# Kernel tuning notes

Hardware: AMD Instinct MI355X
Metric: run time of the kernel (lower is better)

## Reference

```python
import jax, jax.numpy as jnp
import numpy as np

NUM_MODELS = 4
B = 16384
HIDDEN = 512
QDIM = 256
LAST_HIDDEN = 256
UW = 0.1          # uncertainty_weight
EPS = 1e-5        # LayerNorm eps (torch default)
FEAT_DIMS = [1024, 768, 512, 640]


def _linear(x, W, b):
    return x @ W.T + b


def _layernorm(h, g, b):
    mu = jnp.mean(h, axis=-1, keepdims=True)
    var = jnp.mean((h - mu) ** 2, axis=-1, keepdims=True)
    return (h - mu) * jax.lax.rsqrt(var + EPS) * g + b


def setup_inputs() -> dict:
    key = jax.random.key(0)
    ks = jax.random.split(key, 40)
    inp = {}
    for i, d in enumerate(FEAT_DIMS):
        inp[f"feat{i}"] = jax.random.normal(ks[i], (B, d), jnp.float32)
        inp[f"W_intra{i}"] = jax.random.normal(ks[4 + i], (HIDDEN, d), jnp.float32) / np.sqrt(d)
        inp[f"b_intra{i}"] = jnp.zeros((HIDDEN,), jnp.float32)
    inp["pred_scores"] = jax.random.uniform(ks[8], (B, NUM_MODELS), jnp.float32)
    inp["pred_vars"] = jax.random.uniform(ks[9], (B, NUM_MODELS), jnp.float32)
    inp["ln_g"] = jnp.ones((HIDDEN,), jnp.float32)
    inp["ln_b"] = jnp.zeros((HIDDEN,), jnp.float32)
    inp["Wq"] = jax.random.normal(ks[10], (QDIM, HIDDEN), jnp.float32) / np.sqrt(HIDDEN)
    inp["bq"] = jnp.zeros((QDIM,), jnp.float32)
    inp["Wk"] = jax.random.normal(ks[11], (QDIM, HIDDEN), jnp.float32) / np.sqrt(HIDDEN)
    inp["bk"] = jnp.zeros((QDIM,), jnp.float32)
    inp["Wv"] = jax.random.normal(ks[12], (QDIM, HIDDEN), jnp.float32) / np.sqrt(HIDDEN)
    inp["bv"] = jnp.zeros((QDIM,), jnp.float32)
    d1 = NUM_MODELS * QDIM + NUM_MODELS
    inp["W1"] = jax.random.normal(ks[13], (LAST_HIDDEN, d1), jnp.float32) / np.sqrt(d1)
    inp["b1"] = jnp.zeros((LAST_HIDDEN,), jnp.float32)
    inp["Wfc"] = jax.random.normal(ks[14], (1, LAST_HIDDEN), jnp.float32) / np.sqrt(LAST_HIDDEN)
    inp["bfc"] = jnp.zeros((1,), jnp.float32)
    return inp


def _forward(feats, pred_scores, pred_vars, W_intras, b_intras,
             ln_g, ln_b, Wq, bq, Wk, bk, Wv, bv, W1, b1, Wfc, bfc):
    # per-model branch: Linear -> ReLU -> (dropout=id) -> ReLU -> LayerNorm
    hiddens = []
    for i in range(NUM_MODELS):
        h = jax.nn.relu(_linear(feats[i], W_intras[i], b_intras[i]))
        h = jax.nn.relu(h)  # second relu after dropout (identity in eval)
        hiddens.append(_layernorm(h, ln_g, ln_b))
    H = jnp.stack(hiddens, axis=1)  # (B, M, HIDDEN)

    # cross-attention with uncertainty; NOTE source bug: key = drop(q) => keys == queries
    q = jnp.einsum('bmh,qh->bmq', H, Wq) + bq          # (B, M, Q)
    k = q                                              # faithful to `key = self.drop(q)`
    v = jnp.einsum('bmh,qh->bmq', H, Wv) + bv          # (B, M, Q)

    scores = jnp.einsum('biq,bjq->bij', q, k)          # (B, M, M)
    vars_ = pred_vars[:, None, :] + pred_vars[:, :, None]  # vars[b,i,j] = v[b,j] + v[b,i]
    scores = jax.nn.softmax(scores - UW * vars_, axis=-1)
    z = jnp.einsum('bij,bjq->biq', scores, v).reshape(B, NUM_MODELS * QDIM)

    out = jnp.concatenate([z, pred_scores], axis=-1)
    out = _linear(out, W1, b1)
    logits = _linear(out, Wfc, bfc)
    return jax.nn.sigmoid(logits)  # (B, 1)


def reference(feat0, feat1, feat2, feat3,
              W_intra0, b_intra0, W_intra1, b_intra1,
              W_intra2, b_intra2, W_intra3, b_intra3,
              pred_scores, pred_vars, ln_g, ln_b,
              Wq, bq, Wk, bk, Wv, bv, W1, b1, Wfc, bfc):
    feats = [feat0, feat1, feat2, feat3]
    W_intras = [W_intra0, W_intra1, W_intra2, W_intra3]
    b_intras = [b_intra0, b_intra1, b_intra2, b_intra3]
    return _forward(feats, pred_scores, pred_vars, W_intras, b_intras,
                    ln_g, ln_b, Wq, bq, Wk, bk, Wv, bv, W1, b1, Wfc, bfc)
```

## Files before the change

kernel.cpp:

```cpp
#include <hip/hip_runtime.h>
#include <hip/hip_bf16.h>


typedef __bf16 bf16;
typedef __bf16 bf16x4_t __attribute__((ext_vector_type(4)));
typedef __bf16 bf16x8_t __attribute__((ext_vector_type(8)));
typedef float  f32x4_t  __attribute__((ext_vector_type(4)));

__device__ __forceinline__ bf16x8_t cvt8(f32x4_t a, f32x4_t b) {
  bf16x8_t r;
  r[0] = (bf16)a[0]; r[1] = (bf16)a[1]; r[2] = (bf16)a[2]; r[3] = (bf16)a[3];
  r[4] = (bf16)b[0]; r[5] = (bf16)b[1]; r[6] = (bf16)b[2]; r[7] = (bf16)b[3];
  return r;
}

__device__ __forceinline__ void gl_lds16(const void* g, void* l) {
  __builtin_amdgcn_global_load_lds(
      (const __attribute__((address_space(1))) void*)g,
      (__attribute__((address_space(3))) void*)l, 16, 0, 0);
}

__device__ __forceinline__ bf16x8_t frag_read(const bf16* Ts, int row, int c0) {
  const int byte = row * 64 + ((c0 ^ ((row >> 1) & 3)) << 4);
  return *(const bf16x8_t*)((const char*)Ts + byte);
}

__device__ __forceinline__ void stage_b16(const bf16* __restrict__ src, int ld,
                                          int k0, bf16* lds) {
  const int l = threadIdx.x & 63;
  const int w = threadIdx.x >> 6;
#pragma unroll
  for (int j = 0; j < 2; ++j) {
    const int rb = w * 32 + j * 16;
    const int r  = rb + (l >> 2);
    const int sc = (l & 3) ^ ((r >> 1) & 3);
    gl_lds16(src + (size_t)r * ld + k0 + sc * 8, (char*)lds + rb * 64);
  }
}

__device__ __forceinline__ void stage_b512(const bf16* __restrict__ src, int ld,
                                           int k0, bf16* lds) {
  const int l = threadIdx.x & 63;
  const int w = threadIdx.x >> 6;
#pragma unroll
  for (int j = 0; j < 8; ++j) {
    const int rb = w * 128 + j * 16;
    const int r  = rb + (l >> 2);
    const int sc = (l & 3) ^ ((r >> 1) & 3);
    gl_lds16(src + (size_t)r * ld + k0 + sc * 8, (char*)lds + rb * 64);
  }
}

__device__ __forceinline__ void commit2(const f32x4_t v[4], bf16* lds,
                                        int srow, int shalf) {
  const int sw = (srow >> 1) & 3;
  *(bf16x8_t*)((char*)lds + srow * 64 + (((shalf * 2)     ^ sw) << 4)) = cvt8(v[0], v[1]);
  *(bf16x8_t*)((char*)lds + srow * 64 + (((shalf * 2 + 1) ^ sw) << 4)) = cvt8(v[2], v[3]);
}

__device__ __forceinline__ void mfma_step(const bf16* As, const bf16* Bs,
                                          f32x4_t acc[4][4]) {
  const int lane = threadIdx.x & 63;
  const int wid  = threadIdx.x >> 6;
  const int wm = wid >> 1, wn = wid & 1;
  const int fr = lane & 15, c0 = lane >> 4;
  bf16x8_t ar[4], br[4];
#pragma unroll
  for (int mi = 0; mi < 4; ++mi) ar[mi] = frag_read(As, wm * 64 + mi * 16 + fr, c0);
#pragma unroll
  for (int ni = 0; ni < 4; ++ni) br[ni] = frag_read(Bs, wn * 64 + ni * 16 + fr, c0);
#pragma unroll
  for (int mi = 0; mi < 4; ++mi)
#pragma unroll
    for (int ni = 0; ni < 4; ++ni)
      acc[mi][ni] = __builtin_amdgcn_mfma_f32_16x16x32_bf16(ar[mi], br[ni], acc[mi][ni], 0, 0, 0);
}

__device__ __forceinline__ void mfma_step8(const bf16* As, const bf16* Bs,
                                           f32x4_t acc[4][8]) {
  const int lane = threadIdx.x & 63;
  const int wn   = threadIdx.x >> 6;
  const int fr = lane & 15, c0 = lane >> 4;
  bf16x8_t ar[4], br[8];
#pragma unroll
  for (int mi = 0; mi < 4; ++mi) ar[mi] = frag_read(As, mi * 16 + fr, c0);
#pragma unroll
  for (int ni = 0; ni < 8; ++ni) br[ni] = frag_read(Bs, wn * 128 + ni * 16 + fr, c0);
#pragma unroll
  for (int mi = 0; mi < 4; ++mi)
#pragma unroll
    for (int ni = 0; ni < 8; ++ni)
      acc[mi][ni] = __builtin_amdgcn_mfma_f32_16x16x32_bf16(ar[mi], br[ni], acc[mi][ni], 0, 0, 0);
}

#define WAIT_VM6()  asm volatile("s_waitcnt vmcnt(6)" ::: "memory")
#define WAIT_VM10() asm volatile("s_waitcnt vmcnt(10)" ::: "memory")
#define WAIT_VM0()  asm volatile("s_waitcnt vmcnt(0)" ::: "memory")
#define WAIT_LGKM() asm volatile("s_waitcnt lgkmcnt(0)" ::: "memory")
#define SBAR()      __builtin_amdgcn_s_barrier()
#define SCHED0()    __builtin_amdgcn_sched_barrier(0)

template<int REG_IS_A>
__device__ __forceinline__ void core_db(
    const float* __restrict__ regsrc, int rld,
    const bf16* __restrict__ dmasrc, int dld, int K,
    bf16* R0, bf16* R1, bf16* D0, bf16* D1, f32x4_t acc[4][4])
{
  const int tid  = threadIdx.x;
  const int srow = tid >> 1, shalf = tid & 1;
  const float* Rf = regsrc + (size_t)srow * rld + shalf * 16;

  f32x4_t ra[4], rb[4];
#pragma unroll
  for (int i = 0; i < 4; ++i) ra[i] = *(const f32x4_t*)(Rf + i * 4);
  stage_b16(dmasrc, dld, 0, D0);

  for (int k0 = 0; k0 < K; k0 += 64) {
    stage_b16(dmasrc, dld, k0 + 32, D1);
#pragma unroll
    for (int i = 0; i < 4; ++i) rb[i] = *(const f32x4_t*)(Rf + k0 + 32 + i * 4);
    WAIT_VM6();
    commit2(ra, R0, srow, shalf);
    WAIT_LGKM();
    SBAR(); SCHED0();
    if (REG_IS_A) mfma_step(R0, D0, acc); else mfma_step(D0, R0, acc);
    SCHED0(); SBAR();
    if (k0 + 64 < K) {
      stage_b16(dmasrc, dld, k0 + 64, D0);
#pragma unroll
      for (int i = 0; i < 4; ++i) ra[i] = *(const f32x4_t*)(Rf + k0 + 64 + i * 4);
      WAIT_VM6();
    } else {
      WAIT_VM0();
    }
    commit2(rb, R1, srow, shalf);
    WAIT_LGKM();
    SBAR(); SCHED0();
    if (REG_IS_A) mfma_step(R1, D1, acc); else mfma_step(D1, R1, acc);
    SCHED0(); SBAR();
  }
}

template<int RELU>
__device__ __forceinline__ void epi_bf16(f32x4_t acc[4][4], bf16* __restrict__ C, int ldc,
                                         const float* __restrict__ bias) {
  const int lane = threadIdx.x & 63;
  const int wid  = threadIdx.x >> 6;
  const int wm = wid >> 1, wn = wid & 1;
  const int fr = lane & 15;
  const int rb = wm * 64 + 4 * (lane >> 4);
  const int cb = wn * 64 + fr;
  float bv[4];
#pragma unroll
  for (int ni = 0; ni < 4; ++ni) bv[ni] = bias[cb + ni * 16];
#pragma unroll
  for (int mi = 0; mi < 4; ++mi)
#pragma unroll
    for (int j = 0; j < 4; ++j)
#pragma unroll
      for (int ni = 0; ni < 4; ++ni) {
        float val = acc[mi][ni][j] + bv[ni];
        if (RELU) val = fmaxf(val, 0.f);
        C[(size_t)(rb + mi * 16 + j) * ldc + cb + ni * 16] = (bf16)val;
      }
}

__device__ __forceinline__ void cp8(bf16* d, const float* s) {
  f32x4_t x0 = *(const f32x4_t*)s;
  f32x4_t x1 = *(const f32x4_t*)(s + 4);
  *(bf16x8_t*)d = cvt8(x0, x1);
}

__global__ __launch_bounds__(256) void prep_kernel(
    const float* __restrict__ w0, const float* __restrict__ w1s,
    const float* __restrict__ w2, const float* __restrict__ w3,
    bf16* __restrict__ o0, bf16* __restrict__ o1,
    bf16* __restrict__ o2, bf16* __restrict__ o3) {
  const int t = blockIdx.x * 256 + threadIdx.x;
  if (t < 65536)       { size_t i = (size_t)t * 8;            cp8(o0 + i, w0 + i); }
  else if (t < 114688) { size_t i = (size_t)(t - 65536) * 8;  cp8(o1 + i, w1s + i); }
  else if (t < 147456) { size_t i = (size_t)(t - 114688) * 8; cp8(o2 + i, w2 + i); }
  else                 { size_t i = (size_t)(t - 147456) * 8; cp8(o3 + i, w3 + i); }
}

__global__ __launch_bounds__(256, 2) void intra_ln_kernel(
    const float* __restrict__ f0, const float* __restrict__ f1,
    const float* __restrict__ f2, const float* __restrict__ f3,
    const bf16* __restrict__ wb0, const bf16* __restrict__ wb1,
    const bf16* __restrict__ wb2, const bf16* __restrict__ wb3,
    const float* __restrict__ bb0, const float* __restrict__ bb1,
    const float* __restrict__ bb2, const float* __restrict__ bb3,
    const float* __restrict__ lng, const float* __restrict__ lnb,
    bf16* __restrict__ Hout) {
  __shared__ __align__(16) char smem[73728];
  bf16* B0 = (bf16*)smem;
  bf16* B1 = (bf16*)(smem + 32768);
  bf16* A0 = (bf16*)(smem + 65536);
  bf16* A1 = (bf16*)(smem + 69632);
  bf16* hl = (bf16*)smem;

  const int bid = blockIdx.x;
  const int lid = (bid & 7) * 128 + (bid >> 3);
  const int z = lid & 3;
  const int y = lid >> 2;
  const float* fp; const bf16* wp; const float* bp; int K;
  switch (z) {
    case 0:  fp = f0; wp = wb0; bp = bb0; K = 1024; break;
    case 1:  fp = f1; wp = wb1; bp = bb1; K = 768;  break;
    case 2:  fp = f2; wp = wb2; bp = bb2; K = 512;  break;
    default: fp = f3; wp = wb3; bp = bb3; K = 640;  break;
  }
  const int tid  = threadIdx.x;
  const int lane = tid & 63;
  const int wn   = tid >> 6;
  const int srow = tid >> 2, sq = tid & 3;
  const float* Af = fp + (size_t)(y * 64 + srow) * K + sq * 8;
  const int abyte = srow * 64 + ((sq ^ ((srow >> 1) & 3)) << 4);

  f32x4_t acc[4][8];
#pragma unroll
  for (int i = 0; i < 4; ++i)
#pragma unroll
    for (int j = 0; j < 8; ++j) acc[i][j] = (f32x4_t){0.f, 0.f, 0.f, 0.f};

  f32x4_t ra0, ra1, rb0, rb1;
  ra0 = *(const f32x4_t*)(Af + 0);  ra1 = *(const f32x4_t*)(Af + 4);
  stage_b512(wp, K, 0, B0);

  for (int k0 = 0; k0 < K; k0 += 64) {
    stage_b512(wp, K, k0 + 32, B1);
    rb0 = *(const f32x4_t*)(Af + k0 + 32);  rb1 = *(const f32x4_t*)(Af + k0 + 36);
    WAIT_VM10();
    { f32x4_t v[1]; (void)v; }
    *(bf16x8_t*)((char*)A0 + abyte) = cvt8(ra0, ra1);
    WAIT_LGKM();
    SBAR(); SCHED0();
    mfma_step8(A0, B0, acc);
    SCHED0(); SBAR();
    if (k0 + 64 < K) {
      stage_b512(wp, K, k0 + 64, B0);
      ra0 = *(const f32x4_t*)(Af + k0 + 64);  ra1 = *(const f32x4_t*)(Af + k0 + 68);
      WAIT_VM10();
    } else {
      WAIT_VM0();
    }
    *(bf16x8_t*)((char*)A1 + abyte) = cvt8(rb0, rb1);
    WAIT_LGKM();
    SBAR(); SCHED0();
    mfma_step8(A1, B1, acc);
    SCHED0(); SBAR();
  }

  const int fr = lane & 15;
  const int rbase = 4 * (lane >> 4);
  const int cb = wn * 128 + fr;
  float bv[8];
#pragma unroll
  for (int ni = 0; ni < 8; ++ni) bv[ni] = bp[cb + ni * 16];
#pragma unroll
  for (int mi = 0; mi < 4; ++mi)
#pragma unroll
    for (int j = 0; j < 4; ++j) {
      const int row = mi * 16 + rbase + j;
#pragma unroll
      for (int ni = 0; ni < 8; ++ni) {
        float v = fmaxf(acc[mi][ni][j] + bv[ni], 0.f);
        hl[row * 512 + cb + ni * 16] = (bf16)v;
      }
    }
  __syncthreads();

  f32x4_t g0 = *(const f32x4_t*)(lng + lane * 8);
  f32x4_t g1 = *(const f32x4_t*)(lng + lane * 8 + 4);
  f32x4_t be0 = *(const f32x4_t*)(lnb + lane * 8);
  f32x4_t be1 = *(const f32x4_t*)(lnb + lane * 8 + 4);
#pragma unroll
  for (int r16 = 0; r16 < 16; ++r16) {
    const int row = wn * 16 + r16;
    const bf16x8_t xv = *(const bf16x8_t*)(hl + row * 512 + lane * 8);
    float xf[8]; float s = 0.f, s2 = 0.f;
#pragma unroll
    for (int j = 0; j < 8; ++j) { xf[j] = (float)xv[j]; s += xf[j]; s2 += xf[j] * xf[j]; }
#pragma unroll
    for (int off = 1; off < 64; off <<= 1) { s += __shfl_xor(s, off); s2 += __shfl_xor(s2, off); }
    const float mu  = s * (1.f / 512.f);
    const float var = s2 * (1.f / 512.f) - mu * mu;
    const float inv = rsqrtf(var + 1e-5f);
    bf16x8_t o;
#pragma unroll
    for (int j = 0; j < 4; ++j) o[j]     = (bf16)((xf[j] - mu) * inv * g0[j] + be0[j]);
#pragma unroll
    for (int j = 0; j < 4; ++j) o[4 + j] = (bf16)((xf[4 + j] - mu) * inv * g1[j] + be1[j]);
    *(bf16x8_t*)(Hout + (size_t)(y * 64 + row) * 2048 + z * 512 + lane * 8) = o;
  }
}

__global__ __launch_bounds__(256) void qv_kernel(
    const bf16* __restrict__ H, const float* __restrict__ Wq,
    const float* __restrict__ Wv, const float* __restrict__ bq,
    const float* __restrict__ bv, bf16* __restrict__ qvout) {
  __shared__ bf16 A0[128 * 32], A1[128 * 32], B0[128 * 32], B1[128 * 32];
  const int bid = blockIdx.x;
  const int lid = (bid & 7) * 256 + (bid >> 3);
  const int x = lid & 3, y = lid >> 2;
  const float* Wsrc = (x < 2) ? Wq : Wv;
  f32x4_t acc[4][4];
#pragma unroll
  for (int i = 0; i < 4; ++i)
#pragma unroll
    for (int j = 0; j < 4; ++j) acc[i][j] = (f32x4_t){0.f, 0.f, 0.f, 0.f};
  core_db<0>(Wsrc + (size_t)((x & 1) * 128) * 512, 512,
             H + (size_t)(y * 128) * 512, 512, 512, B0, B1, A0, A1, acc);
  const float* bias = (x < 2) ? bq + x * 128 : bv + (x - 2) * 128;
  epi_bf16<0>(acc, qvout + (size_t)(y * 128) * 512 + x * 128, 512, bias);
}

__global__ __launch_bounds__(256) void w1_kernel(
    const bf16* __restrict__ zb, const float* __restrict__ W1,
    const float* __restrict__ b1, const float* __restrict__ ps,
    float* __restrict__ obuf) {
  __shared__ bf16 A0[128 * 32], A1[128 * 32], B0[128 * 32], B1[128 * 32];
  const int bid = blockIdx.x;
  const int lid = (bid & 7) * 32 + (bid >> 3);
  const int x = lid & 1, y = lid >> 1;
  f32x4_t acc[4][4];
#pragma unroll
  for (int i = 0; i < 4; ++i)
#pragma unroll
    for (int j = 0; j < 4; ++j) acc[i][j] = (f32x4_t){0.f, 0.f, 0.f, 0.f};
  core_db<0>(W1 + (size_t)(x * 128) * 1028, 1028,
             zb + (size_t)(y * 128) * 1024, 1024, 1024, B0, B1, A0, A1, acc);

  const int lane = threadIdx.x & 63;
  const int wid  = threadIdx.x >> 6;
  const int wm = wid >> 1, wn = wid & 1;
  const int fr = lane & 15;
  const int rb = wm * 64 + 4 * (lane >> 4);
  const int cb = x * 128 + wn * 64 + fr;
  float bv[4], wt[4][4];
#pragma unroll
  for (int ni = 0; ni < 4; ++ni) {
    bv[ni] = b1[cb + ni * 16];
#pragma unroll
    for (int m = 0; m < 4; ++m) wt[ni][m] = W1[(size_t)(cb + ni * 16) * 1028 + 1024 + m];
  }
#pragma unroll
  for (int mi = 0; mi < 4; ++mi)
#pragma unroll
    for (int j = 0; j < 4; ++j) {
      const int r = y * 128 + rb + mi * 16 + j;
      f32x4_t psv = *(const f32x4_t*)(ps + (size_t)r * 4);
#pragma unroll
      for (int ni = 0; ni < 4; ++ni) {
        float val = acc[mi][ni][j] + bv[ni]
                  + psv[0] * wt[ni][0] + psv[1] * wt[ni][1]
                  + psv[2] * wt[ni][2] + psv[3] * wt[ni][3];
        obuf[(size_t)r * 256 + cb + ni * 16] = val;
      }
    }
}

__global__ __launch_bounds__(256)
void attn_kernel(const bf16* __restrict__ qv, const float* __restrict__ pvars,
                 bf16* __restrict__ z) {
  const int b    = blockIdx.x * 4 + (threadIdx.x >> 6);
  const int lane = threadIdx.x & 63;
  float qf[4][4], vf[4][4];
#pragma unroll
  for (int i = 0; i < 4; ++i) {
    const bf16* row = qv + ((size_t)b * 4 + i) * 512;
    bf16x4_t qq = *(const bf16x4_t*)(row + lane * 4);
    bf16x4_t vv = *(const bf16x4_t*)(row + 256 + lane * 4);
#pragma unroll
    for (int c = 0; c < 4; ++c) { qf[i][c] = (float)qq[c]; vf[i][c] = (float)vv[c]; }
  }
  float s[4][4];
#pragma unroll
  for (int i = 0; i < 4; ++i)
#pragma unroll
    for (int j = 0; j < 4; ++j)
      s[i][j] = qf[i][0] * qf[j][0] + qf[i][1] * qf[j][1] + qf[i][2] * qf[j][2] + qf[i][3] * qf[j][3];
#pragma unroll
  for (int off = 1; off < 64; off <<= 1)
#pragma unroll
    for (int i = 0; i < 4; ++i)
#pragma unroll
      for (int j = 0; j < 4; ++j) s[i][j] += __shfl_xor(s[i][j], off);

  float var4[4];
#pragma unroll
  for (int m = 0; m < 4; ++m) var4[m] = pvars[(size_t)b * 4 + m];
  float w[4][4];
#pragma unroll
  for (int i = 0; i < 4; ++i) {
    float t[4]; float mx = -1e30f;
#pragma unroll
    for (int j = 0; j < 4; ++j) { t[j] = s[i][j] - 0.1f * (var4[i] + var4[j]); mx = fmaxf(mx, t[j]); }
    float sum = 0.f;
#pragma unroll
    for (int j = 0; j < 4; ++j) { t[j] = expf(t[j] - mx); sum += t[j]; }
    const float is = 1.f / sum;
#pragma unroll
    for (int j = 0; j < 4; ++j) w[i][j] = t[j] * is;
  }
#pragma unroll
  for (int i = 0; i < 4; ++i) {
    bf16x4_t zo;
#pragma unroll
    for (int c = 0; c < 4; ++c) {
      float zf = w[i][0] * vf[0][c] + w[i][1] * vf[1][c] + w[i][2] * vf[2][c] + w[i][3] * vf[3][c];
      zo[c] = (bf16)zf;
    }
    *(bf16x4_t*)(z + ((size_t)b * 4 + i) * 256 + lane * 4) = zo;
  }
}

__global__ __launch_bounds__(256)
void fc_kernel(const float* __restrict__ o, const float* __restrict__ wfc,
               const float* __restrict__ bfc, float* __restrict__ out) {
  const int b    = blockIdx.x * 4 + (threadIdx.x >> 6);
  const int lane = threadIdx.x & 63;
  f32x4_t ov = *(const f32x4_t*)(o + (size_t)b * 256 + lane * 4);
  f32x4_t wv = *(const f32x4_t*)(wfc + lane * 4);
  float p = ov[0] * wv[0] + ov[1] * wv[1] + ov[2] * wv[2] + ov[3] * wv[3];
#pragma unroll
  for (int off = 1; off < 64; off <<= 1) p += __shfl_xor(p, off);
  if (lane == 0) {
    const float lg = p + bfc[0];
    out[b] = 1.f / (1.f + expf(-lg));
  }
}

extern "C" void kernel_launch(void* const* d_in, const int* in_sizes, int n_in,
                              void* d_out, int out_size, void* d_ws, size_t ws_size,
                              hipStream_t stream) {
  (void)in_sizes; (void)n_in; (void)out_size; (void)ws_size;
  const float* feat[4] = {(const float*)d_in[0], (const float*)d_in[3],
                          (const float*)d_in[6], (const float*)d_in[9]};
  const float* Wi[4]   = {(const float*)d_in[1], (const float*)d_in[4],
                          (const float*)d_in[7], (const float*)d_in[10]};
  const float* bi[4]   = {(const float*)d_in[2], (const float*)d_in[5],
                          (const float*)d_in[8], (const float*)d_in[11]};
  const float* ps  = (const float*)d_in[12];
  const float* pv  = (const float*)d_in[13];
  const float* lng = (const float*)d_in[14];
  const float* lnb = (const float*)d_in[15];
  const float* Wq  = (const float*)d_in[16];
  const float* bq  = (const float*)d_in[17];
  const float* Wv  = (const float*)d_in[20];
  const float* bvp = (const float*)d_in[21];
  const float* W1  = (const float*)d_in[22];
  const float* b1  = (const float*)d_in[23];
  const float* Wfc = (const float*)d_in[24];
  const float* bfc = (const float*)d_in[25];

  char* ws = (char*)d_ws;
  const size_t MB = 1024 * 1024;
  bf16*  Hbuf  = (bf16*)ws;
  bf16*  zbuf  = (bf16*)ws;
  float* obuf  = (float*)(ws + 32 * MB);
  bf16*  wb0   = (bf16*)(ws + 64 * MB);
  bf16*  wb1   = (bf16*)(ws + 65 * MB);
  bf16*  wb2   = (bf16*)(ws + 65 * MB + 786432);
  bf16*  wb3   = (bf16*)(ws + 66 * MB + 262144);
  bf16*  qvout = (bf16*)(ws + 64 * MB);

  hipLaunchKernelGGL(prep_kernel, dim3(736), dim3(256), 0, stream,
                     Wi[0], Wi[1], Wi[2], Wi[3], wb0, wb1, wb2, wb3);
  hipLaunchKernelGGL(intra_ln_kernel, dim3(1024), dim3(256), 0, stream,
                     feat[0], feat[1], feat[2], feat[3],
                     wb0, wb1, wb2, wb3, bi[0], bi[1], bi[2], bi[3],
                     lng, lnb, Hbuf);
  hipLaunchKernelGGL(qv_kernel, dim3(2048), dim3(256), 0, stream,
                     Hbuf, Wq, Wv, bq, bvp, qvout);
  hipLaunchKernelGGL(attn_kernel, dim3(16384 / 4), dim3(256), 0, stream, qvout, pv, zbuf);
  hipLaunchKernelGGL(w1_kernel, dim3(256), dim3(256), 0, stream, zbuf, W1, b1, ps, obuf);
  hipLaunchKernelGGL(fc_kernel, dim3(16384 / 4), dim3(256), 0, stream, obuf, Wfc, bfc, (float*)d_out);
}
```

Measured before the change: 255.4 us.

## Fuse Q/V projection into intra-branch LayerNorm kernel with register-held B fragments

Merges the per-model linear+ReLU+LayerNorm kernel with the Q/V projection so the normalized hidden tile stays in LDS (XOR-swizzled) and is consumed directly as the A operand, removing the H round trip through global memory and one launch. The B operand (weights) is now loaded straight from global into registers instead of being staged through LDS, shrinking shared memory. Wq/Wv are pre-converted to bf16 in the prep kernel. Risks include higher register pressure with two sets of B fragments, uncoalesced-ish direct global B loads, and a longer serial kernel per block.

```diff
diff --git a/kernel.cpp b/kernel.cpp
--- a/kernel.cpp
+++ b/kernel.cpp
@@ -25,144 +25,49 @@
   return *(const bf16x8_t*)((const char*)Ts + byte);
 }
 
-__device__ __forceinline__ void stage_b16(const bf16* __restrict__ src, int ld,
-                                          int k0, bf16* lds) {
-  const int l = threadIdx.x & 63;
-  const int w = threadIdx.x >> 6;
-#pragma unroll
-  for (int j = 0; j < 2; ++j) {
-    const int rb = w * 32 + j * 16;
-    const int r  = rb + (l >> 2);
-    const int sc = (l & 3) ^ ((r >> 1) & 3);
-    gl_lds16(src + (size_t)r * ld + k0 + sc * 8, (char*)lds + rb * 64);
-  }
-}
-
-__device__ __forceinline__ void stage_b512(const bf16* __restrict__ src, int ld,
-                                           int k0, bf16* lds) {
-  const int l = threadIdx.x & 63;
-  const int w = threadIdx.x >> 6;
-#pragma unroll
-  for (int j = 0; j < 8; ++j) {
-    const int rb = w * 128 + j * 16;
-    const int r  = rb + (l >> 2);
-    const int sc = (l & 3) ^ ((r >> 1) & 3);
-    gl_lds16(src + (size_t)r * ld + k0 + sc * 8, (char*)lds + rb * 64);
-  }
-}
-
-__device__ __forceinline__ void commit2(const f32x4_t v[4], bf16* lds,
-                                        int srow, int shalf) {
-  const int sw = (srow >> 1) & 3;
-  *(bf16x8_t*)((char*)lds + srow * 64 + (((shalf * 2)     ^ sw) << 4)) = cvt8(v[0], v[1]);
-  *(bf16x8_t*)((char*)lds + srow * 64 + (((shalf * 2 + 1) ^ sw) << 4)) = cvt8(v[2], v[3]);
-}
-
-__device__ __forceinline__ void mfma_step(const bf16* As, const bf16* Bs,
-                                          f32x4_t acc[4][4]) {
-  const int lane = threadIdx.x & 63;
-  const int wid  = threadIdx.x >> 6;
-  const int wm = wid >> 1, wn = wid & 1;
-  const int fr = lane & 15, c0 = lane >> 4;
-  bf16x8_t ar[4], br[4];
-#pragma unroll
-  for (int mi = 0; mi < 4; ++mi) ar[mi] = frag_read(As, wm * 64 + mi * 16 + fr, c0);
-#pragma unroll
-  for (int ni = 0; ni < 4; ++ni) br[ni] = frag_read(Bs, wn * 64 + ni * 16 + fr, c0);
-#pragma unroll
-  for (int mi = 0; mi < 4; ++mi)
-#pragma unroll
-    for (int ni = 0; ni < 4; ++ni)
-      acc[mi][ni] = __builtin_amdgcn_mfma_f32_16x16x32_bf16(ar[mi], br[ni], acc[mi][ni], 0, 0, 0);
-}
-
-__device__ __forceinline__ void mfma_step8(const bf16* As, const bf16* Bs,
-                                           f32x4_t acc[4][8]) {
-  const int lane = threadIdx.x & 63;
-  const int wn   = threadIdx.x >> 6;
-  const int fr = lane & 15, c0 = lane >> 4;
-  bf16x8_t ar[4], br[8];
-#pragma unroll
-  for (int mi = 0; mi < 4; ++mi) ar[mi] = frag_read(As, mi * 16 + fr, c0);
-#pragma unroll
-  for (int ni = 0; ni < 8; ++ni) br[ni] = frag_read(Bs, wn * 128 + ni * 16 + fr, c0);
-#pragma unroll
-  for (int mi = 0; mi < 4; ++mi)
-#pragma unroll
-    for (int ni = 0; ni < 8; ++ni)
-      acc[mi][ni] = __builtin_amdgcn_mfma_f32_16x16x32_bf16(ar[mi], br[ni], acc[mi][ni], 0, 0, 0);
-}
-
 #define WAIT_VM6()  asm volatile("s_waitcnt vmcnt(6)" ::: "memory")
-#define WAIT_VM10() asm volatile("s_waitcnt vmcnt(10)" ::: "memory")
 #define WAIT_VM0()  asm volatile("s_waitcnt vmcnt(0)" ::: "memory")
 #define WAIT_LGKM() asm volatile("s_waitcnt lgkmcnt(0)" ::: "memory")
 #define SBAR()      __builtin_amdgcn_s_barrier()
 #define SCHED0()    __builtin_amdgcn_sched_barrier(0)
 
-template<int REG_IS_A>
-__device__ __forceinline__ void core_db(
-    const float* __restrict__ regsrc, int rld,
-    const bf16* __restrict__ dmasrc, int dld, int K,
-    bf16* R0, bf16* R1, bf16* D0, bf16* D1, f32x4_t acc[4][4])
-{
-  const int tid  = threadIdx.x;
-  const int srow = tid >> 1, shalf = tid & 1;
-  const float* Rf = regsrc + (size_t)srow * rld + shalf * 16;
-
-  f32x4_t ra[4], rb[4];
-#pragma unroll
-  for (int i = 0; i < 4; ++i) ra[i] = *(const f32x4_t*)(Rf + i * 4);
-  stage_b16(dmasrc, dld, 0, D0);
-
-  for (int k0 = 0; k0 < K; k0 += 64) {
-    stage_b16(dmasrc, dld, k0 + 32, D1);
-#pragma unroll
-    for (int i = 0; i < 4; ++i) rb[i] = *(const f32x4_t*)(Rf + k0 + 32 + i * 4);
-    WAIT_VM6();
-    commit2(ra, R0, srow, shalf);
-    WAIT_LGKM();
-    SBAR(); SCHED0();
-    if (REG_IS_A) mfma_step(R0, D0, acc); else mfma_step(D0, R0, acc);
-    SCHED0(); SBAR();
-    if (k0 + 64 < K) {
-      stage_b16(dmasrc, dld, k0 + 64, D0);
-#pragma unroll
-      for (int i = 0; i < 4; ++i) ra[i] = *(const f32x4_t*)(Rf + k0 + 64 + i * 4);
-      WAIT_VM6();
-    } else {
-      WAIT_VM0();
-    }
-    commit2(rb, R1, srow, shalf);
-    WAIT_LGKM();
-    SBAR(); SCHED0();
-    if (REG_IS_A) mfma_step(R1, D1, acc); else mfma_step(D1, R1, acc);
-    SCHED0(); SBAR();
-  }
-}
-
-template<int RELU>
-__device__ __forceinline__ void epi_bf16(f32x4_t acc[4][4], bf16* __restrict__ C, int ldc,
-                                         const float* __restrict__ bias) {
-  const int lane = threadIdx.x & 63;
-  const int wid  = threadIdx.x >> 6;
-  const int wm = wid >> 1, wn = wid & 1;
-  const int fr = lane & 15;
-  const int rb = wm * 64 + 4 * (lane >> 4);
-  const int cb = wn * 64 + fr;
-  float bv[4];
-#pragma unroll
-  for (int ni = 0; ni < 4; ++ni) bv[ni] = bias[cb + ni * 16];
+__device__ __forceinline__ void loadB8(const bf16* __restrict__ base, int ld,
+                                       int k0, bf16x8_t br[8]) {
+#pragma unroll
+  for (int ni = 0; ni < 8; ++ni)
+    br[ni] = *(const bf16x8_t*)(base + (size_t)ni * 16 * ld + k0);
+}
+
+__device__ __forceinline__ void mfma_regB(const bf16* As, const bf16x8_t br[8],
+                                          f32x4_t acc[4][8]) {
+  const int lane = threadIdx.x & 63;
+  const int fr = lane & 15, c0 = lane >> 4;
+  bf16x8_t ar[4];
+#pragma unroll
+  for (int mi = 0; mi < 4; ++mi) ar[mi] = frag_read(As, mi * 16 + fr, c0);
 #pragma unroll
   for (int mi = 0; mi < 4; ++mi)
 #pragma unroll
-    for (int j = 0; j < 4; ++j)
-#pragma unroll
-      for (int ni = 0; ni < 4; ++ni) {
-        float val = acc[mi][ni][j] + bv[ni];
-        if (RELU) val = fmaxf(val, 0.f);
-        C[(size_t)(rb + mi * 16 + j) * ldc + cb + ni * 16] = (bf16)val;
-      }
+    for (int ni = 0; ni < 8; ++ni)
+      acc[mi][ni] = __builtin_amdgcn_mfma_f32_16x16x32_bf16(ar[mi], br[ni], acc[mi][ni], 0, 0, 0);
+}
+
+__device__ __forceinline__ void mfma_hA(const bf16* h, int kc, const bf16x8_t br[8],
+                                        f32x4_t acc[4][8]) {
+  const int lane = threadIdx.x & 63;
+  const int fr = lane & 15, g = lane >> 4;
+  bf16x8_t ar[4];
+#pragma unroll
+  for (int mi = 0; mi < 4; ++mi) {
+    const int row = mi * 16 + fr;
+    const int byte = row * 1024 + (((kc + g) ^ (row & 7)) << 4);
+    ar[mi] = *(const bf16x8_t*)((const char*)h + byte);
+  }
+#pragma unroll
+  for (int mi = 0; mi < 4; ++mi)
+#pragma unroll
+    for (int ni = 0; ni < 8; ++ni)
+      acc[mi][ni] = __builtin_amdgcn_mfma_f32_16x16x32_bf16(ar[mi], br[ni], acc[mi][ni], 0, 0, 0);
 }
 
 __device__ __forceinline__ void cp8(bf16* d, const float* s) {
@@ -174,16 +79,19 @@
 __global__ __launch_bounds__(256) void prep_kernel(
     const float* __restrict__ w0, const float* __restrict__ w1s,
     const float* __restrict__ w2, const float* __restrict__ w3,
-    bf16* __restrict__ o0, bf16* __restrict__ o1,
-    bf16* __restrict__ o2, bf16* __restrict__ o3) {
+    const float* __restrict__ wq, const float* __restrict__ wv,
+    bf16* __restrict__ o0, bf16* __restrict__ o1, bf16* __restrict__ o2,
+    bf16* __restrict__ o3, bf16* __restrict__ oqv) {
   const int t = blockIdx.x * 256 + threadIdx.x;
   if (t < 65536)       { size_t i = (size_t)t * 8;            cp8(o0 + i, w0 + i); }
   else if (t < 114688) { size_t i = (size_t)(t - 65536) * 8;  cp8(o1 + i, w1s + i); }
   else if (t < 147456) { size_t i = (size_t)(t - 114688) * 8; cp8(o2 + i, w2 + i); }
-  else                 { size_t i = (size_t)(t - 147456) * 8; cp8(o3 + i, w3 + i); }
-}
-
-__global__ __launch_bounds__(256, 2) void intra_ln_kernel(
+  else if (t < 188416) { size_t i = (size_t)(t - 147456) * 8; cp8(o3 + i, w3 + i); }
+  else                 { int u = t - 188416; size_t i = (size_t)u * 8;
+                         cp8(oqv + i, (u < 16384) ? wq + i : wv + (i - 131072)); }
+}
+
+__global__ __launch_bounds__(256, 2) void mega_kernel(
     const float* __restrict__ f0, const float* __restrict__ f1,
     const float* __restrict__ f2, const float* __restrict__ f3,
     const bf16* __restrict__ wb0, const bf16* __restrict__ wb1,
@@ -191,13 +99,11 @@
     const float* __restrict__ bb0, const float* __restrict__ bb1,
     const float* __restrict__ bb2, const float* __restrict__ bb3,
     const float* __restrict__ lng, const float* __restrict__ lnb,
-    bf16* __restrict__ Hout) {
-  __shared__ __align__(16) char smem[73728];
-  bf16* B0 = (bf16*)smem;
-  bf16* B1 = (bf16*)(smem + 32768);
-  bf16* A0 = (bf16*)(smem + 65536);
-  bf16* A1 = (bf16*)(smem + 69632);
-  bf16* hl = (bf16*)smem;
+    const bf16* __restrict__ wqv, const float* __restrict__ bq,
+    const float* __restrict__ bv, bf16* __restrict__ qvout) {
+  __shared__ bf16 A0[64 * 32];
+  __shared__ bf16 A1[64 * 32];
+  __shared__ bf16 h[64 * 512];
 
   const int bid = blockIdx.x;
   const int lid = (bid & 7) * 128 + (bid >> 3);
@@ -213,9 +119,11 @@
   const int tid  = threadIdx.x;
   const int lane = tid & 63;
   const int wn   = tid >> 6;
+  const int fr   = lane & 15, g = lane >> 4;
   const int srow = tid >> 2, sq = tid & 3;
   const float* Af = fp + (size_t)(y * 64 + srow) * K + sq * 8;
   const int abyte = srow * 64 + ((sq ^ ((srow >> 1) & 3)) << 4);
+  const bf16* Bbase = wp + (size_t)(wn * 128 + fr) * K + g * 8;
 
   f32x4_t acc[4][8];
 #pragma unroll
@@ -224,95 +132,188 @@
     for (int j = 0; j < 8; ++j) acc[i][j] = (f32x4_t){0.f, 0.f, 0.f, 0.f};
 
   f32x4_t ra0, ra1, rb0, rb1;
+  bf16x8_t bc[8], bn[8];
   ra0 = *(const f32x4_t*)(Af + 0);  ra1 = *(const f32x4_t*)(Af + 4);
-  stage_b512(wp, K, 0, B0);
+  loadB8(Bbase, K, 0, bc);
 
   for (int k0 = 0; k0 < K; k0 += 64) {
-    stage_b512(wp, K, k0 + 32, B1);
+    loadB8(Bbase, K, k0 + 32, bn);
     rb0 = *(const f32x4_t*)(Af + k0 + 32);  rb1 = *(const f32x4_t*)(Af + k0 + 36);
-    WAIT_VM10();
-    { f32x4_t v[1]; (void)v; }
     *(bf16x8_t*)((char*)A0 + abyte) = cvt8(ra0, ra1);
     WAIT_LGKM();
     SBAR(); SCHED0();
-    mfma_step8(A0, B0, acc);
+    mfma_regB(A0, bc, acc);
     SCHED0(); SBAR();
     if (k0 + 64 < K) {
-      stage_b512(wp, K, k0 + 64, B0);
+      loadB8(Bbase, K, k0 + 64, bc);
       ra0 = *(const f32x4_t*)(Af + k0 + 64);  ra1 = *(const f32x4_t*)(Af + k0 + 68);
-      WAIT_VM10();
-    } else {
-      WAIT_VM0();
     }
     *(bf16x8_t*)((char*)A1 + abyte) = cvt8(rb0, rb1);
     WAIT_LGKM();
     SBAR(); SCHED0();
-    mfma_step8(A1, B1, acc);
+    mfma_regB(A1, bn, acc);
     SCHED0(); SBAR();
   }
 
-  const int fr = lane & 15;
-  const int rbase = 4 * (lane >> 4);
-  const int cb = wn * 128 + fr;
-  float bv[8];
-#pragma unroll
-  for (int ni = 0; ni < 8; ++ni) bv[ni] = bp[cb + ni * 16];
+  const int g4 = 4 * g;
+  {
+    float bv8[8];
+#pragma unroll
+    for (int ni = 0; ni < 8; ++ni) bv8[ni] = bp[wn * 128 + ni * 16 + fr];
+#pragma unroll
+    for (int mi = 0; mi < 4; ++mi)
+#pragma unroll
+      for (int j = 0; j < 4; ++j) {
+        const int row = mi * 16 + g4 + j;
+#pragma unroll
+        for (int ni = 0; ni < 8; ++ni) {
+          const int col = wn * 128 + ni * 16 + fr;
+          const int hb = row * 1024 + (((col >> 3) ^ (row & 7)) << 4) + (col & 7) * 2;
+          float v = fmaxf(acc[mi][ni][j] + bv8[ni], 0.f);
+          *(bf16*)((char*)h + hb) = (bf16)v;
+        }
+      }
+  }
+  __syncthreads();
+
+  {
+    f32x4_t gg0 = *(const f32x4_t*)(lng + lane * 8);
+    f32x4_t gg1 = *(const f32x4_t*)(lng + lane * 8 + 4);
+    f32x4_t be0 = *(const f32x4_t*)(lnb + lane * 8);
+    f32x4_t be1 = *(const f32x4_t*)(lnb + lane * 8 + 4);
+#pragma unroll
+    for (int r16 = 0; r16 < 16; ++r16) {
+      const int row = wn * 16 + r16;
+      const int hb = row * 1024 + ((lane ^ (row & 7)) << 4);
+      const bf16x8_t xv = *(const bf16x8_t*)((const char*)h + hb);
+      float xf[8]; float s = 0.f, s2 = 0.f;
+#pragma unroll
+      for (int j = 0; j < 8; ++j) { xf[j] = (float)xv[j]; s += xf[j]; s2 += xf[j] * xf[j]; }
+#pragma unroll
+      for (int off = 1; off < 64; off <<= 1) { s += __shfl_xor(s, off); s2 += __shfl_xor(s2, off); }
+      const float mu  = s * (1.f / 512.f);
+      const float var = s2 * (1.f / 512.f) - mu * mu;
+      const float inv = rsqrtf(var + 1e-5f);
+      bf16x8_t o;
+#pragma unroll
+      for (int j = 0; j < 4; ++j) o[j]     = (bf16)((xf[j] - mu) * inv * gg0[j] + be0[j]);
+#pragma unroll
+      for (int j = 0; j < 4; ++j) o[4 + j] = (bf16)((xf[4 + j] - mu) * inv * gg1[j] + be1[j]);
+      *(bf16x8_t*)((char*)h + hb) = o;
+    }
+  }
+  __syncthreads();
+
+#pragma unroll
+  for (int i = 0; i < 4; ++i)
+#pragma unroll
+    for (int j = 0; j < 8; ++j) acc[i][j] = (f32x4_t){0.f, 0.f, 0.f, 0.f};
+  const bf16* Qbase = wqv + (size_t)(wn * 128 + fr) * 512 + g * 8;
+  bf16x8_t qc[8], qn[8];
+  loadB8(Qbase, 512, 0, qc);
+  for (int k0 = 0; k0 < 512; k0 += 64) {
+    loadB8(Qbase, 512, k0 + 32, qn);
+    mfma_hA(h, k0 >> 3, qc, acc);
+    if (k0 + 64 < 512) loadB8(Qbase, 512, k0 + 64, qc);
+    mfma_hA(h, (k0 + 32) >> 3, qn, acc);
+  }
+
+  {
+    float bv8[8];
+#pragma unroll
+    for (int ni = 0; ni < 8; ++ni) {
+      const int col = wn * 128 + ni * 16 + fr;
+      bv8[ni] = (col < 256) ? bq[col] : bv[col - 256];
+    }
+#pragma unroll
+    for (int mi = 0; mi < 4; ++mi)
+#pragma unroll
+      for (int j = 0; j < 4; ++j) {
+        const int row = mi * 16 + g4 + j;
+        bf16* outp = qvout + ((size_t)(y * 64 + row) * 4 + z) * 512;
+#pragma unroll
+        for (int ni = 0; ni < 8; ++ni) {
+          const int col = wn * 128 + ni * 16 + fr;
+          outp[col] = (bf16)(acc[mi][ni][j] + bv8[ni]);
+        }
+      }
+  }
+}
+
+__device__ __forceinline__ void stage_b16(const bf16* __restrict__ src, int ld,
+                                          int k0, bf16* lds) {
+  const int l = threadIdx.x & 63;
+  const int w = threadIdx.x >> 6;
+#pragma unroll
+  for (int j = 0; j < 2; ++j) {
+    const int rb = w * 32 + j * 16;
+    const int r  = rb + (l >> 2);
+    const int sc = (l & 3) ^ ((r >> 1) & 3);
+    gl_lds16(src + (size_t)r * ld + k0 + sc * 8, (char*)lds + rb * 64);
+  }
+}
+
+__device__ __forceinline__ void commit2(const f32x4_t v[4], bf16* lds,
+                                        int srow, int shalf) {
+  const int sw = (srow >> 1) & 3;
+  *(bf16x8_t*)((char*)lds + srow * 64 + (((shalf * 2)     ^ sw) << 4)) = cvt8(v[0], v[1]);
+  *(bf16x8_t*)((char*)lds + srow * 64 + (((shalf * 2 + 1) ^ sw) << 4)) = cvt8(v[2], v[3]);
+}
+
+__device__ __forceinline__ void mfma_step(const bf16* As, const bf16* Bs,
+                                          f32x4_t acc[4][4]) {
+  const int lane = threadIdx.x & 63;
+  const int wid  = threadIdx.x >> 6;
+  const int wm = wid >> 1, wn = wid & 1;
+  const int fr = lane & 15, c0 = lane >> 4;
+  bf16x8_t ar[4], br[4];
+#pragma unroll
+  for (int mi = 0; mi < 4; ++mi) ar[mi] = frag_read(As, wm * 64 + mi * 16 + fr, c0);
+#pragma unroll
+  for (int ni = 0; ni < 4; ++ni) br[ni] = frag_read(Bs, wn * 64 + ni * 16 + fr, c0);
 #pragma unroll
   for (int mi = 0; mi < 4; ++mi)
 #pragma unroll
-    for (int j = 0; j < 4; ++j) {
-      const int row = mi * 16 + rbase + j;
-#pragma unroll
-      for (int ni = 0; ni < 8; ++ni) {
-        float v = fmaxf(acc[mi][ni][j] + bv[ni], 0.f);
-        hl[row * 512 + cb + ni * 16] = (bf16)v;
-      }
-    }
-  __syncthreads();
-
-  f32x4_t g0 = *(const f32x4_t*)(lng + lane * 8);
-  f32x4_t g1 = *(const f32x4_t*)(lng + lane * 8 + 4);
-  f32x4_t be0 = *(const f32x4_t*)(lnb + lane * 8);
-  f32x4_t be1 = *(const f32x4_t*)(lnb + lane * 8 + 4);
-#pragma unroll
-  for (int r16 = 0; r16 < 16; ++r16) {
-    const int row = wn * 16 + r16;
-    const bf16x8_t xv = *(const bf16x8_t*)(hl + row * 512 + lane * 8);
-    float xf[8]; float s = 0.f, s2 = 0.f;
-#pragma unroll
-    for (int j = 0; j < 8; ++j) { xf[j] = (float)xv[j]; s += xf[j]; s2 += xf[j] * xf[j]; }
-#pragma unroll
-    for (int off = 1; off < 64; off <<= 1) { s += __shfl_xor(s, off); s2 += __shfl_xor(s2, off); }
-    const float mu  = s * (1.f / 512.f);
-    const float var = s2 * (1.f / 512.f) - mu * mu;
-    const float inv = rsqrtf(var + 1e-5f);
-    bf16x8_t o;
-#pragma unroll
-    for (int j = 0; j < 4; ++j) o[j]     = (bf16)((xf[j] - mu) * inv * g0[j] + be0[j]);
-#pragma unroll
-    for (int j = 0; j < 4; ++j) o[4 + j] = (bf16)((xf[4 + j] - mu) * inv * g1[j] + be1[j]);
-    *(bf16x8_t*)(Hout + (size_t)(y * 64 + row) * 2048 + z * 512 + lane * 8) = o;
-  }
-}
-
-__global__ __launch_bounds__(256) void qv_kernel(
-    const bf16* __restrict__ H, const float* __restrict__ Wq,
-    const float* __restrict__ Wv, const float* __restrict__ bq,
-    const float* __restrict__ bv, bf16* __restrict__ qvout) {
-  __shared__ bf16 A0[128 * 32], A1[128 * 32], B0[128 * 32], B1[128 * 32];
-  const int bid = blockIdx.x;
-  const int lid = (bid & 7) * 256 + (bid >> 3);
-  const int x = lid & 3, y = lid >> 2;
-  const float* Wsrc = (x < 2) ? Wq : Wv;
-  f32x4_t acc[4][4];
-#pragma unroll
-  for (int i = 0; i < 4; ++i)
-#pragma unroll
-    for (int j = 0; j < 4; ++j) acc[i][j] = (f32x4_t){0.f, 0.f, 0.f, 0.f};
-  core_db<0>(Wsrc + (size_t)((x & 1) * 128) * 512, 512,
-             H + (size_t)(y * 128) * 512, 512, 512, B0, B1, A0, A1, acc);
-  const float* bias = (x < 2) ? bq + x * 128 : bv + (x - 2) * 128;
-  epi_bf16<0>(acc, qvout + (size_t)(y * 128) * 512 + x * 128, 512, bias);
+    for (int ni = 0; ni < 4; ++ni)
+      acc[mi][ni] = __builtin_amdgcn_mfma_f32_16x16x32_bf16(ar[mi], br[ni], acc[mi][ni], 0, 0, 0);
+}
+
+__device__ __forceinline__ void core_db0(
+    const float* __restrict__ regsrc, int rld,
+    const bf16* __restrict__ dmasrc, int dld, int K,
+    bf16* R0, bf16* R1, bf16* D0, bf16* D1, f32x4_t acc[4][4])
+{
+  const int tid  = threadIdx.x;
+  const int srow = tid >> 1, shalf = tid & 1;
+  const float* Rf = regsrc + (size_t)srow * rld + shalf * 16;
+  f32x4_t ra[4], rb[4];
+#pragma unroll
+  for (int i = 0; i < 4; ++i) ra[i] = *(const f32x4_t*)(Rf + i * 4);
+  stage_b16(dmasrc, dld, 0, D0);
+  for (int k0 = 0; k0 < K; k0 += 64) {
+    stage_b16(dmasrc, dld, k0 + 32, D1);
+#pragma unroll
+    for (int i = 0; i < 4; ++i) rb[i] = *(const f32x4_t*)(Rf + k0 + 32 + i * 4);
+    WAIT_VM6();
+    commit2(ra, R0, srow, shalf);
+    WAIT_LGKM();
+    SBAR(); SCHED0();
+    mfma_step(D0, R0, acc);
+    SCHED0(); SBAR();
+    if (k0 + 64 < K) {
+      stage_b16(dmasrc, dld, k0 + 64, D0);
+#pragma unroll
+      for (int i = 0; i < 4; ++i) ra[i] = *(const f32x4_t*)(Rf + k0 + 64 + i * 4);
+      WAIT_VM6();
+    } else {
+      WAIT_VM0();
+    }
+    commit2(rb, R1, srow, shalf);
+    WAIT_LGKM();
+    SBAR(); SCHED0();
+    mfma_step(D1, R1, acc);
+    SCHED0(); SBAR();
+  }
 }
 
 __global__ __launch_bounds__(256) void w1_kernel(
@@ -328,8 +329,8 @@
   for (int i = 0; i < 4; ++i)
 #pragma unroll
     for (int j = 0; j < 4; ++j) acc[i][j] = (f32x4_t){0.f, 0.f, 0.f, 0.f};
-  core_db<0>(W1 + (size_t)(x * 128) * 1028, 1028,
-             zb + (size_t)(y * 128) * 1024, 1024, 1024, B0, B1, A0, A1, acc);
+  core_db0(W1 + (size_t)(x * 128) * 1028, 1028,
+           zb + (size_t)(y * 128) * 1024, 1024, 1024, B0, B1, A0, A1, acc);
 
   const int lane = threadIdx.x & 63;
   const int wid  = threadIdx.x >> 6;
@@ -456,23 +457,22 @@
 
   char* ws = (char*)d_ws;
   const size_t MB = 1024 * 1024;
-  bf16*  Hbuf  = (bf16*)ws;
-  bf16*  zbuf  = (bf16*)ws;
-  float* obuf  = (float*)(ws + 32 * MB);
-  bf16*  wb0   = (bf16*)(ws + 64 * MB);
-  bf16*  wb1   = (bf16*)(ws + 65 * MB);
-  bf16*  wb2   = (bf16*)(ws + 65 * MB + 786432);
-  bf16*  wb3   = (bf16*)(ws + 66 * MB + 262144);
+  bf16*  wb0   = (bf16*)(ws);
+  bf16*  wb1   = (bf16*)(ws + 1048576);
+  bf16*  wb2   = (bf16*)(ws + 1835008);
+  bf16*  wb3   = (bf16*)(ws + 2359296);
+  bf16*  wqv   = (bf16*)(ws + 3014656);
+  bf16*  zbuf  = (bf16*)(ws + 8 * MB);
+  float* obuf  = (float*)(ws + 40 * MB);
   bf16*  qvout = (bf16*)(ws + 64 * MB);
 
-  hipLaunchKernelGGL(prep_kernel, dim3(736), dim3(256), 0, stream,
-                     Wi[0], Wi[1], Wi[2], Wi[3], wb0, wb1, wb2, wb3);
-  hipLaunchKernelGGL(intra_ln_kernel, dim3(1024), dim3(256), 0, stream,
+  hipLaunchKernelGGL(prep_kernel, dim3(864), dim3(256), 0, stream,
+                     Wi[0], Wi[1], Wi[2], Wi[3], Wq, Wv,
+                     wb0, wb1, wb2, wb3, wqv);
+  hipLaunchKernelGGL(mega_kernel, dim3(1024), dim3(256), 0, stream,
                      feat[0], feat[1], feat[2], feat[3],
                      wb0, wb1, wb2, wb3, bi[0], bi[1], bi[2], bi[3],
-                     lng, lnb, Hbuf);
-  hipLaunchKernelGGL(qv_kernel, dim3(2048), dim3(256), 0, stream,
-                     Hbuf, Wq, Wv, bq, bvp, qvout);
+                     lng, lnb, wqv, bq, bvp, qvout);
   hipLaunchKernelGGL(attn_kernel, dim3(16384 / 4), dim3(256), 0, stream, qvout, pv, zbuf);
   hipLaunchKernelGGL(w1_kernel, dim3(256), dim3(256), 0, stream, zbuf, W1, b1, ps, obuf);
   hipLaunchKernelGGL(fc_kernel, dim3(16384 / 4), dim3(256), 0, stream, obuf, Wfc, bfc, (float*)d_out);
```

New measurement: 288.5 us. +12.9%, slower.
